# Performance work log

Measured on AMD Instinct MI355X. Metric: run time of the kernel, lower is better.

Reference implementation:

```python
import jax, jax.numpy as jnp
import numpy as np

NEG_SLOPE = 0.2


def _add_self_loops(src, dst, edge_attr, n):
    # PyG add_self_loops with fill_value='mean': self-loop attr for node i is the
    # mean of edge_attr over edges whose target is i (0 if none).
    attr_sum = jax.ops.segment_sum(edge_attr, dst, num_segments=n)          # [N,1]
    cnt = jax.ops.segment_sum(jnp.ones((src.shape[0],), edge_attr.dtype), dst, num_segments=n)
    loop_attr = attr_sum / jnp.maximum(cnt, 1.0)[:, None]                   # [N,1]
    loop = jnp.arange(n, dtype=src.dtype)
    return (jnp.concatenate([src, loop]),
            jnp.concatenate([dst, loop]),
            jnp.concatenate([edge_attr, loop_attr], axis=0))


def _gatv2_layer(x, src, dst, eattr, Wl, Wr, We, att, b, n):
    # GATv2Conv (heads=1, concat=False): e_ij = att . leaky_relu(Wl x_j + Wr x_i + We a_ij)
    xl = x @ Wl                                   # [N,C] source transform
    xr = x @ Wr                                   # [N,C] target transform
    ef = eattr @ We                               # [E,C]
    z = jax.nn.leaky_relu(xl[src] + xr[dst] + ef, NEG_SLOPE)   # [E,C]
    logits = z @ att                              # [E]
    # segment softmax over target node dst
    m = jax.ops.segment_max(logits, dst, num_segments=n)
    ex = jnp.exp(logits - m[dst])
    s = jax.ops.segment_sum(ex, dst, num_segments=n)
    alpha = ex / (s[dst] + 1e-16)                 # [E]
    out = jax.ops.segment_sum(alpha[:, None] * xl[src], dst, num_segments=n)  # [N,C]
    return out + b


def setup_inputs() -> dict:
    key = jax.random.key(0)
    ks = jax.random.split(key, 16)
    N, E, F_IN, H, OUT = 50000, 800000, 128, 128, 64
    x = jax.random.normal(ks[0], (N, F_IN), jnp.float32)
    edge_index = jax.random.randint(ks[1], (2, E), 0, N, jnp.int32)
    edge_attr = jax.random.normal(ks[2], (E, 1), jnp.float32)
    s = 0.1
    return {
        "x": x, "edge_index": edge_index, "edge_attr": edge_attr,
        "Wl1": jax.random.normal(ks[3], (F_IN, H), jnp.float32) * s,
        "Wr1": jax.random.normal(ks[4], (F_IN, H), jnp.float32) * s,
        "We1": jax.random.normal(ks[5], (1, H), jnp.float32) * s,
        "att1": jax.random.normal(ks[6], (H,), jnp.float32) * s,
        "b1": jnp.zeros((H,), jnp.float32),
        "Wl2": jax.random.normal(ks[7], (H, OUT), jnp.float32) * s,
        "Wr2": jax.random.normal(ks[8], (H, OUT), jnp.float32) * s,
        "We2": jax.random.normal(ks[9], (1, OUT), jnp.float32) * s,
        "att2": jax.random.normal(ks[10], (OUT,), jnp.float32) * s,
        "b2": jnp.zeros((OUT,), jnp.float32),
    }


def reference(x, edge_index, edge_attr, Wl1, Wr1, We1, att1, b1, Wl2, Wr2, We2, att2, b2):
    n = x.shape[0]
    src, dst, ea = _add_self_loops(edge_index[0], edge_index[1], edge_attr, n)
    h = jax.nn.elu(_gatv2_layer(x, src, dst, ea, Wl1, Wr1, We1, att1, b1, n))
    out = jax.nn.elu(_gatv2_layer(h, src, dst, ea, Wl2, Wr2, We2, att2, b2, n))
    return out
```

## Files before the change

kernel.cpp:

```cpp
#include <hip/hip_runtime.h>
#include <math.h>


#define NEG_SLOPE 0.2f
#define CNT_SHIFT 44
#define SUM_MASK ((1ULL << 44) - 1)
#define ATTR_BIAS 8.0
#define ATTR_SCALE 268435456.0

typedef __attribute__((ext_vector_type(8))) short bf16x8;
typedef __attribute__((ext_vector_type(4))) float f32x4;

__device__ __forceinline__ float bf_lo(unsigned int u) { return __uint_as_float(u << 16); }
__device__ __forceinline__ float bf_hi(unsigned int u) { return __uint_as_float(u & 0xFFFF0000u); }
__device__ __forceinline__ unsigned short bf16_rne(float f) {
    unsigned int u = __float_as_uint(f);
    return (unsigned short)((u + 0x7FFFu + ((u >> 16) & 1u)) >> 16);
}
__device__ __forceinline__ unsigned int pack_bf16(float a, float b) {
    unsigned int ua = __float_as_uint(a);
    unsigned int ub = __float_as_uint(b);
    ua = (ua + 0x7FFFu + ((ua >> 16) & 1u)) >> 16;
    ub = (ub + 0x7FFFu + ((ub >> 16) & 1u)) & 0xFFFF0000u;
    return ua | ub;
}

__global__ void wprep_kernel(const float* __restrict__ Wl1, const float* __restrict__ Wr1,
                             const float* __restrict__ Wl2, const float* __restrict__ Wr2,
                             short* __restrict__ Wt1, short* __restrict__ Wt2) {
    int i = blockIdx.x * 256 + threadIdx.x;
    if (i < 256 * 128) {
        int nn = i >> 7, k = i & 127;
        float v = (nn < 128) ? Wl1[k * 128 + nn] : Wr1[k * 128 + (nn - 128)];
        Wt1[i] = (short)bf16_rne(v);
    } else if (i < 256 * 128 + 128 * 128) {
        int j = i - 256 * 128;
        int nn = j >> 7, k = j & 127;
        float v = (nn < 64) ? Wl2[k * 64 + nn] : Wr2[k * 64 + (nn - 64)];
        Wt2[j] = (short)bf16_rne(v);
    }
}

__global__ void edge_pass1_kernel(const int* __restrict__ dst, const float* __restrict__ eattr,
                                  unsigned long long* __restrict__ packed,
                                  unsigned short* __restrict__ rank, int E) {
    int e = blockIdx.x * blockDim.x + threadIdx.x;
    if (e < E) {
        int d = dst[e];
        double q = ((double)eattr[e] + ATTR_BIAS) * ATTR_SCALE;
        unsigned long long inc = (1ULL << CNT_SHIFT) | (unsigned long long)q;
        unsigned long long old = atomicAdd(&packed[d], inc);
        rank[e] = (unsigned short)(old >> CNT_SHIFT);
    }
}

__global__ __launch_bounds__(1024) void scan_part_kernel(
    const unsigned long long* __restrict__ packed, int* __restrict__ partials, int n) {
    __shared__ int red[1024];
    int gid = blockIdx.x * 1024 + threadIdx.x;
    red[threadIdx.x] = (gid < n) ? ((int)(packed[gid] >> CNT_SHIFT) + 1) : 0;
    __syncthreads();
    for (int off = 512; off > 0; off >>= 1) {
        if (threadIdx.x < off) red[threadIdx.x] += red[threadIdx.x + off];
        __syncthreads();
    }
    if (threadIdx.x == 0) partials[blockIdx.x] = red[0];
}

__global__ __launch_bounds__(1024) void scan_blocksums_kernel(int* __restrict__ partials, int nb) {
    __shared__ int buf[1024];
    int t = threadIdx.x;
    int v = (t < nb) ? partials[t] : 0;
    buf[t] = v;
    __syncthreads();
    for (int off = 1; off < 1024; off <<= 1) {
        int a = (t >= off) ? buf[t - off] : 0;
        __syncthreads();
        buf[t] += a;
        __syncthreads();
    }
    if (t < nb) partials[t] = buf[t] - v;
}

__global__ __launch_bounds__(1024) void scan_final_kernel(
    const unsigned long long* __restrict__ packed, const int* __restrict__ partials,
    int* __restrict__ row_ptr, int n) {
    __shared__ int buf[1024];
    int gid = blockIdx.x * 1024 + threadIdx.x;
    int v = (gid < n) ? ((int)(packed[gid] >> CNT_SHIFT) + 1) : 0;
    buf[threadIdx.x] = v;
    __syncthreads();
    for (int off = 1; off < 1024; off <<= 1) {
        int a = (threadIdx.x >= off) ? buf[threadIdx.x - off] : 0;
        __syncthreads();
        buf[threadIdx.x] += a;
        __syncthreads();
    }
    if (gid < n) row_ptr[gid + 1] = partials[blockIdx.x] + buf[threadIdx.x];
    if (gid == 0) row_ptr[0] = 0;
}

__global__ void csr_scatter_kernel(const int* __restrict__ src, const int* __restrict__ dst,
                                   const float* __restrict__ eattr,
                                   const unsigned long long* __restrict__ packed,
                                   const unsigned short* __restrict__ rank,
                                   const int* __restrict__ row_ptr,
                                   int2* __restrict__ csr, int E, int n) {
    int i = blockIdx.x * blockDim.x + threadIdx.x;
    if (i < E) {
        int d = dst[i];
        csr[row_ptr[d] + rank[i]] = make_int2(src[i], __float_as_int(eattr[i]));
    } else if (i < E + n) {
        int v = i - E;
        unsigned long long p = packed[v];
        int cnt = (int)(p >> CNT_SHIFT);
        double sum = (double)(p & SUM_MASK) * (1.0 / ATTR_SCALE) - ATTR_BIAS * cnt;
        float mean = (cnt > 0) ? (float)(sum / cnt) : 0.f;
        csr[row_ptr[v] + cnt] = make_int2(v, __float_as_int(mean));
    }
}

template <int COUT, int WM, int WN>
__global__ __launch_bounds__(256) void xform_mfma_kernel(
    const float* __restrict__ X, const short* __restrict__ Wt,
    unsigned short* __restrict__ XL, float* __restrict__ XR, int n) {
    constexpr int CIN = 128;
    constexpr int BM = WM * 64;
    constexpr int PITCH = CIN + 8;
    static_assert(WM * WN == 4, "4 waves");
    __shared__ short xs[BM * PITCH];

    const int t = threadIdx.x;
    const int node0 = blockIdx.x * BM;

    constexpr int NF4 = BM * CIN / 4;
    const float4* Xv = (const float4*)(X + (size_t)node0 * CIN);
    for (int idx = t; idx < NF4; idx += 256) {
        int r = idx >> 5;
        int c4 = idx & 31;
        uint2 w;
        if (node0 + r < n) {
            float4 v = Xv[idx];
            w = make_uint2(pack_bf16(v.x, v.y), pack_bf16(v.z, v.w));
        } else {
            w = make_uint2(0u, 0u);
        }
        *(uint2*)(xs + r * PITCH + c4 * 4) = w;
    }
    __syncthreads();

    const int wv = t >> 6, lane = t & 63;
    const int mw = wv / WN, nw = wv % WN;
    const int m0 = mw * 64, n0 = nw * 64;
    const int ln = lane & 15, kg = lane >> 4;

    f32x4 acc[4][4];
#pragma unroll
    for (int i = 0; i < 4; ++i)
#pragma unroll
        for (int j = 0; j < 4; ++j) acc[i][j] = (f32x4){0.f, 0.f, 0.f, 0.f};

#pragma unroll
    for (int ks = 0; ks < 4; ++ks) {
        bf16x8 b[4], a[4];
#pragma unroll
        for (int mt = 0; mt < 4; ++mt)
            b[mt] = *(const bf16x8*)(xs + (m0 + mt * 16 + ln) * PITCH + ks * 32 + kg * 8);
#pragma unroll
        for (int nt = 0; nt < 4; ++nt)
            a[nt] = *(const bf16x8*)(Wt + (size_t)(n0 + nt * 16 + ln) * CIN + ks * 32 + kg * 8);
#pragma unroll
        for (int nt = 0; nt < 4; ++nt)
#pragma unroll
            for (int mt = 0; mt < 4; ++mt)
                acc[nt][mt] = __builtin_amdgcn_mfma_f32_16x16x32_bf16(
                    a[nt], b[mt], acc[nt][mt], 0, 0, 0);
    }

    const bool isXL = (n0 < COUT);
#pragma unroll
    for (int mt = 0; mt < 4; ++mt) {
        int m = node0 + m0 + mt * 16 + ln;
        if (m >= n) continue;
#pragma unroll
        for (int nt = 0; nt < 4; ++nt) {
            f32x4 v = acc[nt][mt];
            int nl = n0 + nt * 16 + kg * 4;
            if (isXL) {
                *(uint2*)(XL + (size_t)m * COUT + nl) =
                    make_uint2(pack_bf16(v.x, v.y), pack_bf16(v.z, v.w));
            } else {
                *(f32x4*)(XR + (size_t)m * COUT + (nl - COUT)) = v;
            }
        }
    }
}

template <int C, int LPE, int U>
__global__ __launch_bounds__(256) void agg_grouped_kernel(
    const unsigned short* __restrict__ XL, const float* XR,
    const int* __restrict__ row_ptr, const int2* __restrict__ csr,
    const float* __restrict__ We, const float* __restrict__ att,
    const float* __restrict__ bias, float* OUT, int n) {
    constexpr int NGRP = 64 / LPE;
    constexpr int CPL = C / LPE;
    constexpr int NW = CPL / 2;
    const int wave = threadIdx.x >> 6;
    const int lane = threadIdx.x & 63;
    const int lg  = lane & (LPE - 1);
    const int grp = lane / LPE;
    const int cb  = lg * CPL;

    float wev[CPL], atv[CPL], bv[CPL];
#pragma unroll
    for (int j = 0; j < CPL; j += 4) {
        *(float4*)&wev[j] = *(const float4*)(We  + cb + j);
        *(float4*)&atv[j] = *(const float4*)(att + cb + j);
        *(float4*)&bv[j]  = *(const float4*)(bias + cb + j);
    }

    const int stride = gridDim.x * 4;
    for (int node = blockIdx.x * 4 + wave; node < n; node += stride) {
        float xr[CPL];
#pragma unroll
        for (int j = 0; j < CPL; j += 4)
            *(float4*)&xr[j] = *(const float4*)(XR + (size_t)node * C + cb + j);

        const int p0 = row_ptr[node], pe = row_ptr[node + 1];
        float s = 0.f;
        float acc[CPL];
#pragma unroll
        for (int j = 0; j < CPL; ++j) acc[j] = 0.f;

        for (int base = p0 + grp; base < pe; base += NGRP * U) {
            int2 ed[U];
            bool valid[U];
#pragma unroll
            for (int u = 0; u < U; ++u) {
                int p = base + u * NGRP;
                valid[u] = (p < pe);
                ed[u] = csr[valid[u] ? p : (pe - 1)];
            }
            unsigned int uw[U][NW];
#pragma unroll
            for (int u = 0; u < U; ++u) {
                uint4 q = *(const uint4*)(XL + (size_t)ed[u].x * C + cb);
                uw[u][0] = q.x; uw[u][1] = q.y; uw[u][2] = q.z; uw[u][3] = q.w;
            }
#pragma unroll
            for (int u = 0; u < U; ++u) {
                float xl[CPL];
#pragma unroll
                for (int j2 = 0; j2 < NW; ++j2) {
                    xl[2 * j2]     = bf_lo(uw[u][j2]);
                    xl[2 * j2 + 1] = bf_hi(uw[u][j2]);
                }
                float ae = __int_as_float(ed[u].y);
                float part = 0.f;
#pragma unroll
                for (int j = 0; j < CPL; ++j) {
                    float z = fmaf(ae, wev[j], xr[j]) + xl[j];
                    z = fmaxf(z, NEG_SLOPE * z);
                    part = fmaf(atv[j], z, part);
                }
#pragma unroll
                for (int off = 1; off < LPE; off <<= 1)
                    part += __shfl_xor(part, off, 64);
                float w = valid[u] ? __expf(part) : 0.f;
                s += w;
#pragma unroll
                for (int j = 0; j < CPL; ++j) acc[j] = fmaf(w, xl[j], acc[j]);
            }
        }

#pragma unroll
        for (int off = LPE; off < 64; off <<= 1) {
            s += __shfl_xor(s, off, 64);
#pragma unroll
            for (int j = 0; j < CPL; ++j) acc[j] += __shfl_xor(acc[j], off, 64);
        }

        if (grp == 0) {
            float inv = 1.f / (s + 1e-16f);
            float o[CPL];
#pragma unroll
            for (int j = 0; j < CPL; ++j) {
                float v = fmaf(acc[j], inv, bv[j]);
                o[j] = (v > 0.f) ? v : (__expf(v) - 1.f);
            }
#pragma unroll
            for (int j = 0; j < CPL; j += 4)
                *(float4*)(OUT + (size_t)node * C + cb + j) = *(const float4*)&o[j];
        }
    }
}

extern "C" void kernel_launch(void* const* d_in, const int* in_sizes, int n_in,
                              void* d_out, int out_size, void* d_ws, size_t ws_size,
                              hipStream_t stream) {
    const float* x    = (const float*)d_in[0];
    const int*   eidx = (const int*)  d_in[1];
    const float* ea   = (const float*)d_in[2];
    const float* Wl1  = (const float*)d_in[3];
    const float* Wr1  = (const float*)d_in[4];
    const float* We1  = (const float*)d_in[5];
    const float* att1 = (const float*)d_in[6];
    const float* b1   = (const float*)d_in[7];
    const float* Wl2  = (const float*)d_in[8];
    const float* Wr2  = (const float*)d_in[9];
    const float* We2  = (const float*)d_in[10];
    const float* att2 = (const float*)d_in[11];
    const float* b2   = (const float*)d_in[12];

    const int FIN = 128, H = 128, OUTC = 64;
    const int E  = in_sizes[2];
    const int N  = in_sizes[0] / FIN;
    const int EP = E + N;
    const int NB = (N + 1023) / 1024;
    const int* src = eidx;
    const int* dst = eidx + E;

    char* ws = (char*)d_ws;
    size_t off = 0;
    auto alloc = [&](size_t bytes) {
        size_t o = off;
        off += (bytes + 255) & ~(size_t)255;
        return o;
    };
    size_t packed_off = alloc((size_t)N * 8);
    size_t zero_bytes = off;
    size_t rank_off  = alloc((size_t)E * 2);
    size_t rp_off    = alloc((size_t)(N + 1) * 4);
    size_t part_off  = alloc((size_t)NB * 4);
    size_t csr_off   = alloc((size_t)EP * 8);
    size_t wt1_off   = alloc((size_t)256 * 128 * 2);
    size_t wt2_off   = alloc((size_t)128 * 128 * 2);
    size_t xl1_off   = alloc((size_t)N * H * 2);
    size_t xr1_off   = alloc((size_t)N * H * 4);
    size_t xr2_off   = alloc((size_t)N * OUTC * 4);

    unsigned long long* packed = (unsigned long long*)(ws + packed_off);
    unsigned short*     rank   = (unsigned short*)(ws + rank_off);
    int*   rp    = (int*)  (ws + rp_off);
    int*   part  = (int*)  (ws + part_off);
    int2*  csr   = (int2*) (ws + csr_off);
    short* wt1   = (short*)(ws + wt1_off);
    short* wt2   = (short*)(ws + wt2_off);
    unsigned short* xl1 = (unsigned short*)(ws + xl1_off);
    float* xr1   = (float*)(ws + xr1_off);
    float* h     = xr1;
    unsigned short* xl2 = (unsigned short*)(ws + xl1_off);
    float* xr2   = (float*)(ws + xr2_off);

    (void)ws_size; (void)n_in; (void)out_size;

    hipMemsetAsync(ws, 0, zero_bytes, stream);

    const int TB = 256;
    const int AGG_BLOCKS = 2048;
    wprep_kernel<<<192, 256, 0, stream>>>(Wl1, Wr1, Wl2, Wr2, wt1, wt2);
    edge_pass1_kernel<<<(E + TB - 1) / TB, TB, 0, stream>>>(dst, ea, packed, rank, E);
    scan_part_kernel<<<NB, 1024, 0, stream>>>(packed, part, N);
    scan_blocksums_kernel<<<1, 1024, 0, stream>>>(part, NB);
    scan_final_kernel<<<NB, 1024, 0, stream>>>(packed, part, rp, N);
    csr_scatter_kernel<<<(EP + TB - 1) / TB, TB, 0, stream>>>(src, dst, ea, packed, rank,
                                                              rp, csr, E, N);
    xform_mfma_kernel<128, 1, 4><<<(N + 63) / 64, 256, 0, stream>>>(x, wt1, xl1, xr1, N);
    agg_grouped_kernel<128, 16, 4><<<AGG_BLOCKS, 256, 0, stream>>>(xl1, xr1, rp, csr,
                                                                   We1, att1, b1, h, N);
    xform_mfma_kernel<64, 2, 2><<<(N + 127) / 128, 256, 0, stream>>>(h, wt2, xl2, xr2, N);
    agg_grouped_kernel<64, 8, 2><<<AGG_BLOCKS, 256, 0, stream>>>(xl2, xr2, rp, csr,
                                                                 We2, att2, b2, (float*)d_out, N);
}
```

Before: 216.1 us.

## Fuse prep kernels, overlap CSR scatter with xform, add nontemporal hints

Merges weight prep with the edge counting pass, and runs the CSR scatter in the same launch as the first-layer MFMA transform. Together these cut the launch count and let independent work share the GPU. Adds nontemporal loads and stores across the edge, CSR and aggregation paths, and packs each CSR entry as a 64-bit integer. Also changes the aggregation grid size and the layer-2 unroll factor. Per-element nontemporal loads of XR and scalar output stores may replace vectorized float4 accesses, which risks less efficient memory traffic.

```diff
diff --git a/kernel.cpp b/kernel.cpp
--- a/kernel.cpp
+++ b/kernel.cpp
@@ -24,33 +24,39 @@
     ub = (ub + 0x7FFFu + ((ub >> 16) & 1u)) & 0xFFFF0000u;
     return ua | ub;
 }
-
-__global__ void wprep_kernel(const float* __restrict__ Wl1, const float* __restrict__ Wr1,
-                             const float* __restrict__ Wl2, const float* __restrict__ Wr2,
-                             short* __restrict__ Wt1, short* __restrict__ Wt2) {
-    int i = blockIdx.x * 256 + threadIdx.x;
-    if (i < 256 * 128) {
-        int nn = i >> 7, k = i & 127;
-        float v = (nn < 128) ? Wl1[k * 128 + nn] : Wr1[k * 128 + (nn - 128)];
-        Wt1[i] = (short)bf16_rne(v);
-    } else if (i < 256 * 128 + 128 * 128) {
-        int j = i - 256 * 128;
-        int nn = j >> 7, k = j & 127;
-        float v = (nn < 64) ? Wl2[k * 64 + nn] : Wr2[k * 64 + (nn - 64)];
-        Wt2[j] = (short)bf16_rne(v);
-    }
-}
-
-__global__ void edge_pass1_kernel(const int* __restrict__ dst, const float* __restrict__ eattr,
+__device__ __forceinline__ long long pack_edge(int sv, float av) {
+    return (long long)(((unsigned long long)(unsigned int)__float_as_int(av) << 32) |
+                       (unsigned long long)(unsigned int)sv);
+}
+
+__global__ void fused_prep_kernel(const float* __restrict__ Wl1, const float* __restrict__ Wr1,
+                                  const float* __restrict__ Wl2, const float* __restrict__ Wr2,
+                                  short* __restrict__ Wt1, short* __restrict__ Wt2,
+                                  const int* __restrict__ dst, const float* __restrict__ eattr,
                                   unsigned long long* __restrict__ packed,
-                                  unsigned short* __restrict__ rank, int E) {
-    int e = blockIdx.x * blockDim.x + threadIdx.x;
-    if (e < E) {
-        int d = dst[e];
-        double q = ((double)eattr[e] + ATTR_BIAS) * ATTR_SCALE;
-        unsigned long long inc = (1ULL << CNT_SHIFT) | (unsigned long long)q;
-        unsigned long long old = atomicAdd(&packed[d], inc);
-        rank[e] = (unsigned short)(old >> CNT_SHIFT);
+                                  unsigned short* __restrict__ rank, int E, int wblocks) {
+    if ((int)blockIdx.x < wblocks) {
+        int i = blockIdx.x * 256 + threadIdx.x;
+        if (i < 256 * 128) {
+            int nn = i >> 7, k = i & 127;
+            float v = (nn < 128) ? Wl1[k * 128 + nn] : Wr1[k * 128 + (nn - 128)];
+            Wt1[i] = (short)bf16_rne(v);
+        } else if (i < 256 * 128 + 128 * 128) {
+            int j = i - 256 * 128;
+            int nn = j >> 7, k = j & 127;
+            float v = (nn < 64) ? Wl2[k * 64 + nn] : Wr2[k * 64 + (nn - 64)];
+            Wt2[j] = (short)bf16_rne(v);
+        }
+    } else {
+        int e = (blockIdx.x - wblocks) * 256 + threadIdx.x;
+        if (e < E) {
+            int d = __builtin_nontemporal_load(dst + e);
+            float a = __builtin_nontemporal_load(eattr + e);
+            double q = ((double)a + ATTR_BIAS) * ATTR_SCALE;
+            unsigned long long inc = (1ULL << CNT_SHIFT) | (unsigned long long)q;
+            unsigned long long old = atomicAdd(&packed[d], inc);
+            rank[e] = (unsigned short)(old >> CNT_SHIFT);
+        }
     }
 }
 
@@ -100,30 +106,10 @@
     if (gid == 0) row_ptr[0] = 0;
 }
 
-__global__ void csr_scatter_kernel(const int* __restrict__ src, const int* __restrict__ dst,
-                                   const float* __restrict__ eattr,
-                                   const unsigned long long* __restrict__ packed,
-                                   const unsigned short* __restrict__ rank,
-                                   const int* __restrict__ row_ptr,
-                                   int2* __restrict__ csr, int E, int n) {
-    int i = blockIdx.x * blockDim.x + threadIdx.x;
-    if (i < E) {
-        int d = dst[i];
-        csr[row_ptr[d] + rank[i]] = make_int2(src[i], __float_as_int(eattr[i]));
-    } else if (i < E + n) {
-        int v = i - E;
-        unsigned long long p = packed[v];
-        int cnt = (int)(p >> CNT_SHIFT);
-        double sum = (double)(p & SUM_MASK) * (1.0 / ATTR_SCALE) - ATTR_BIAS * cnt;
-        float mean = (cnt > 0) ? (float)(sum / cnt) : 0.f;
-        csr[row_ptr[v] + cnt] = make_int2(v, __float_as_int(mean));
-    }
-}
-
 template <int COUT, int WM, int WN>
-__global__ __launch_bounds__(256) void xform_mfma_kernel(
+__device__ __forceinline__ void xform_body(
     const float* __restrict__ X, const short* __restrict__ Wt,
-    unsigned short* __restrict__ XL, float* __restrict__ XR, int n) {
+    unsigned short* __restrict__ XL, float* __restrict__ XR, int n, int blk) {
     constexpr int CIN = 128;
     constexpr int BM = WM * 64;
     constexpr int PITCH = CIN + 8;
@@ -131,7 +117,7 @@
     __shared__ short xs[BM * PITCH];
 
     const int t = threadIdx.x;
-    const int node0 = blockIdx.x * BM;
+    const int node0 = blk * BM;
 
     constexpr int NF4 = BM * CIN / 4;
     const float4* Xv = (const float4*)(X + (size_t)node0 * CIN);
@@ -196,10 +182,45 @@
     }
 }
 
+__global__ __launch_bounds__(256) void fused_sx_kernel(
+    const float* __restrict__ X, const short* __restrict__ Wt1,
+    unsigned short* __restrict__ XL, float* __restrict__ XR,
+    const int* __restrict__ src, const int* __restrict__ dst,
+    const float* __restrict__ eattr,
+    const unsigned long long* __restrict__ packed,
+    const unsigned short* __restrict__ rank,
+    const int* __restrict__ row_ptr, long long* __restrict__ csr,
+    int E, int n, int xblocks) {
+    if ((int)blockIdx.x < xblocks) {
+        xform_body<128, 1, 4>(X, Wt1, XL, XR, n, blockIdx.x);
+    } else {
+        int i = (blockIdx.x - xblocks) * 256 + threadIdx.x;
+        if (i < E) {
+            int d = __builtin_nontemporal_load(dst + i);
+            int sv = __builtin_nontemporal_load(src + i);
+            float av = __builtin_nontemporal_load(eattr + i);
+            __builtin_nontemporal_store(pack_edge(sv, av), csr + row_ptr[d] + rank[i]);
+        } else if (i < E + n) {
+            int v = i - E;
+            unsigned long long p = packed[v];
+            int cnt = (int)(p >> CNT_SHIFT);
+            double sum = (double)(p & SUM_MASK) * (1.0 / ATTR_SCALE) - ATTR_BIAS * cnt;
+            float mean = (cnt > 0) ? (float)(sum / cnt) : 0.f;
+            __builtin_nontemporal_store(pack_edge(v, mean), csr + row_ptr[v] + cnt);
+        }
+    }
+}
+
+__global__ __launch_bounds__(256) void xform2_kernel(
+    const float* __restrict__ X, const short* __restrict__ Wt,
+    unsigned short* __restrict__ XL, float* __restrict__ XR, int n) {
+    xform_body<64, 2, 2>(X, Wt, XL, XR, n, blockIdx.x);
+}
+
 template <int C, int LPE, int U>
 __global__ __launch_bounds__(256) void agg_grouped_kernel(
     const unsigned short* __restrict__ XL, const float* XR,
-    const int* __restrict__ row_ptr, const int2* __restrict__ csr,
+    const int* __restrict__ row_ptr, const long long* __restrict__ csr,
     const float* __restrict__ We, const float* __restrict__ att,
     const float* __restrict__ bias, float* OUT, int n) {
     constexpr int NGRP = 64 / LPE;
@@ -222,9 +243,11 @@
     const int stride = gridDim.x * 4;
     for (int node = blockIdx.x * 4 + wave; node < n; node += stride) {
         float xr[CPL];
-#pragma unroll
-        for (int j = 0; j < CPL; j += 4)
-            *(float4*)&xr[j] = *(const float4*)(XR + (size_t)node * C + cb + j);
+        {
+            const float* xp = XR + (size_t)node * C + cb;
+#pragma unroll
+            for (int j = 0; j < CPL; ++j) xr[j] = __builtin_nontemporal_load(xp + j);
+        }
 
         const int p0 = row_ptr[node], pe = row_ptr[node + 1];
         float s = 0.f;
@@ -233,18 +256,19 @@
         for (int j = 0; j < CPL; ++j) acc[j] = 0.f;
 
         for (int base = p0 + grp; base < pe; base += NGRP * U) {
-            int2 ed[U];
+            long long ed[U];
             bool valid[U];
 #pragma unroll
             for (int u = 0; u < U; ++u) {
                 int p = base + u * NGRP;
                 valid[u] = (p < pe);
-                ed[u] = csr[valid[u] ? p : (pe - 1)];
+                ed[u] = __builtin_nontemporal_load(csr + (valid[u] ? p : (pe - 1)));
             }
             unsigned int uw[U][NW];
 #pragma unroll
             for (int u = 0; u < U; ++u) {
-                uint4 q = *(const uint4*)(XL + (size_t)ed[u].x * C + cb);
+                int sj = (int)(unsigned int)(ed[u] & 0xFFFFFFFFull);
+                uint4 q = *(const uint4*)(XL + (size_t)sj * C + cb);
                 uw[u][0] = q.x; uw[u][1] = q.y; uw[u][2] = q.z; uw[u][3] = q.w;
             }
 #pragma unroll
@@ -255,7 +279,7 @@
                     xl[2 * j2]     = bf_lo(uw[u][j2]);
                     xl[2 * j2 + 1] = bf_hi(uw[u][j2]);
                 }
-                float ae = __int_as_float(ed[u].y);
+                float ae = __int_as_float((int)((unsigned long long)ed[u] >> 32));
                 float part = 0.f;
 #pragma unroll
                 for (int j = 0; j < CPL; ++j) {
@@ -282,15 +306,13 @@
 
         if (grp == 0) {
             float inv = 1.f / (s + 1e-16f);
-            float o[CPL];
+            float* op = OUT + (size_t)node * C + cb;
 #pragma unroll
             for (int j = 0; j < CPL; ++j) {
                 float v = fmaf(acc[j], inv, bv[j]);
-                o[j] = (v > 0.f) ? v : (__expf(v) - 1.f);
-            }
-#pragma unroll
-            for (int j = 0; j < CPL; j += 4)
-                *(float4*)(OUT + (size_t)node * C + cb + j) = *(const float4*)&o[j];
+                v = (v > 0.f) ? v : (__expf(v) - 1.f);
+                __builtin_nontemporal_store(v, op + j);
+            }
         }
     }
 }
@@ -343,7 +365,7 @@
     unsigned short*     rank   = (unsigned short*)(ws + rank_off);
     int*   rp    = (int*)  (ws + rp_off);
     int*   part  = (int*)  (ws + part_off);
-    int2*  csr   = (int2*) (ws + csr_off);
+    long long* csr = (long long*)(ws + csr_off);
     short* wt1   = (short*)(ws + wt1_off);
     short* wt2   = (short*)(ws + wt2_off);
     unsigned short* xl1 = (unsigned short*)(ws + xl1_off);
@@ -354,21 +376,24 @@
 
     (void)ws_size; (void)n_in; (void)out_size;
 
-    hipMemsetAsync(ws, 0, zero_bytes, stream);
-
-    const int TB = 256;
-    const int AGG_BLOCKS = 2048;
-    wprep_kernel<<<192, 256, 0, stream>>>(Wl1, Wr1, Wl2, Wr2, wt1, wt2);
-    edge_pass1_kernel<<<(E + TB - 1) / TB, TB, 0, stream>>>(dst, ea, packed, rank, E);
+    (void)hipMemsetAsync(ws, 0, zero_bytes, stream);
+
+    const int WPREP_BLOCKS = 192;
+    const int P1_BLOCKS = (E + 255) / 256;
+    const int XF1_BLOCKS = (N + 63) / 64;
+    const int SC_BLOCKS = (EP + 255) / 256;
+    const int AGG_BLOCKS = 1792;
+
+    fused_prep_kernel<<<WPREP_BLOCKS + P1_BLOCKS, 256, 0, stream>>>(
+        Wl1, Wr1, Wl2, Wr2, wt1, wt2, dst, ea, packed, rank, E, WPREP_BLOCKS);
     scan_part_kernel<<<NB, 1024, 0, stream>>>(packed, part, N);
     scan_blocksums_kernel<<<1, 1024, 0, stream>>>(part, NB);
     scan_final_kernel<<<NB, 1024, 0, stream>>>(packed, part, rp, N);
-    csr_scatter_kernel<<<(EP + TB - 1) / TB, TB, 0, stream>>>(src, dst, ea, packed, rank,
-                                                              rp, csr, E, N);
-    xform_mfma_kernel<128, 1, 4><<<(N + 63) / 64, 256, 0, stream>>>(x, wt1, xl1, xr1, N);
+    fused_sx_kernel<<<XF1_BLOCKS + SC_BLOCKS, 256, 0, stream>>>(
+        x, wt1, xl1, xr1, src, dst, ea, packed, rank, rp, csr, E, N, XF1_BLOCKS);
     agg_grouped_kernel<128, 16, 4><<<AGG_BLOCKS, 256, 0, stream>>>(xl1, xr1, rp, csr,
                                                                    We1, att1, b1, h, N);
-    xform_mfma_kernel<64, 2, 2><<<(N + 127) / 128, 256, 0, stream>>>(h, wt2, xl2, xr2, N);
-    agg_grouped_kernel<64, 8, 2><<<AGG_BLOCKS, 256, 0, stream>>>(xl2, xr2, rp, csr,
+    xform2_kernel<<<(N + 127) / 128, 256, 0, stream>>>(h, wt2, xl2, xr2, N);
+    agg_grouped_kernel<64, 8, 4><<<AGG_BLOCKS, 256, 0, stream>>>(xl2, xr2, rp, csr,
                                                                  We2, att2, b2, (float*)d_out, N);
 }
```

Result: slower. 226.4 us (median of 2 runs) (+4.8%).
